# Kernel optimization log

Hardware: AMD Instinct MI355X
Metric: run time of the kernel (lower is better)

The kernel has to match this reference:

```python
import jax, jax.numpy as jnp
import numpy as np

N, M, C, CSKIP, K = 16384, 4096, 256, 128, 3
BIG = 1e10  # distance penalty for cross-batch pairs


def setup_inputs() -> dict:
    key = jax.random.key(0)
    ks = jax.random.split(key, 6)
    return {
        "x": jax.random.normal(ks[0], (M, C), jnp.float32),
        "pos": jax.random.normal(ks[1], (M, 3), jnp.float32),
        "batch": jnp.zeros((M,), jnp.int32),
        "x_skip": jax.random.normal(ks[2], (N, CSKIP), jnp.float32),
        "pos_skip": jax.random.normal(ks[3], (N, 3), jnp.float32),
        "batch_skip": jnp.zeros((N,), jnp.int32),
        "W1": jax.random.normal(ks[4], (C + CSKIP, 256), jnp.float32) * (1.0 / np.sqrt(C + CSKIP)),
        "b1": jnp.zeros((256,), jnp.float32),
        "W2": jax.random.normal(ks[5], (256, 256), jnp.float32) * (1.0 / np.sqrt(256)),
        "b2": jnp.zeros((256,), jnp.float32),
    }


def _knn_idx(pos, pos_skip, batch, batch_skip, k):
    # Squared distances via GEMM form: [N, M]
    a2 = jnp.sum(pos_skip * pos_skip, axis=-1, keepdims=True)      # [N,1]
    b2 = jnp.sum(pos * pos, axis=-1)[None, :]                       # [1,M]
    d2 = a2 + b2 - 2.0 * (pos_skip @ pos.T)                         # [N,M]
    d2 = jnp.where(batch_skip[:, None] != batch[None, :], BIG, d2)
    _, idx = jax.lax.top_k(-d2, k)                                  # [N,k]
    return idx


def reference(x, pos, batch, x_skip, pos_skip, batch_skip, W1, b1, W2, b2):
    idx = _knn_idx(pos, pos_skip, batch, batch_skip, K)             # [N,k] coarse neighbor ids
    # Exact squared dist recomputed from gathered positions (matches torch diff path)
    diff = pos_skip[:, None, :] - pos[idx]                          # [N,k,3]
    d2 = jnp.sum(diff * diff, axis=-1, keepdims=True)               # [N,k,1]
    w = 1.0 / (d2 + 1e-8)                                           # inverse-distance weights
    wsum = jnp.sum(w, axis=1, keepdims=True)                        # per-row scatter_add == sum over k
    w = w / (wsum + 1e-8)
    x_interp = jnp.sum(w * x[idx], axis=1)                          # [N,C]
    h = jnp.concatenate([x_interp, x_skip], axis=1)                 # [N,C+C']
    h = jax.nn.relu(h @ W1 + b1)
    h = jax.nn.relu(h @ W2 + b2)
    return h
```

## Files before the change

### kernel.cpp

```cpp
#include <hip/hip_runtime.h>

typedef float     f4   __attribute__((ext_vector_type(4)));
typedef float     f32x4 __attribute__((ext_vector_type(4)));
typedef _Float16  h8   __attribute__((ext_vector_type(8)));
typedef _Float16  h4   __attribute__((ext_vector_type(4)));
typedef int       i4   __attribute__((ext_vector_type(4)));

#define NQ   16384
#define MP   4096
#define CF   256
#define CSK  128
#define K1   384
#define HID  256
#define QB   16

__global__ __launch_bounds__(256) void wconv_kernel(
    const float* __restrict__ W1, const float* __restrict__ W2,
    _Float16* __restrict__ Wt1, _Float16* __restrict__ Wt2)
{
    const int i = blockIdx.x * 256 + threadIdx.x;
    if (i < K1 * HID) {
        const int k = i >> 8, n = i & 255;
        Wt1[(size_t)(k >> 5) * 8192 + ((k >> 3) & 3) * 2048 + n * 8 + (k & 7)]
            = (_Float16)W1[i];
    } else {
        const int i2 = i - K1 * HID;
        const int k = i2 >> 8, n = i2 & 255;
        Wt2[(size_t)(k >> 5) * 8192 + ((k >> 3) & 3) * 2048 + n * 8 + (k & 7)]
            = (_Float16)W2[i2];
    }
}

__global__ __launch_bounds__(256, 4) void fused_kernel(
    const float* __restrict__ pos,
    const float* __restrict__ pos_skip,
    const float* __restrict__ x,
    const float* __restrict__ x_skip,
    const _Float16* __restrict__ Wt1,
    const _Float16* __restrict__ Wt2,
    const float* __restrict__ b1,
    const float* __restrict__ b2,
    float* __restrict__ out)
{
    __shared__ __align__(16) char smem[26112];
    _Float16* pxh = (_Float16*)smem;
    _Float16* pyh = (_Float16*)(smem + 8192);
    _Float16* pzh = (_Float16*)(smem + 16384);
    unsigned short (*ci)[48] = (unsigned short (*)[48])(smem + 24576);
    int   (*fidx)[3] = (int (*)[3])(smem + 24576);
    float (*fw)[3]   = (float (*)[3])(smem + 24768);
    _Float16 (*As)[392] = (_Float16 (*)[392])smem;
    _Float16 (*Hs)[264] = (_Float16 (*)[264])smem;

    const int tid = threadIdx.x;

    {
        const f4* posv = (const f4*)pos;
        for (int m = tid; m < MP / 4; m += 256) {
            const f4 a = posv[3*m], b = posv[3*m+1], c = posv[3*m+2];
            h4 hx, hy, hz;
            hx[0]=(_Float16)a[0]; hx[1]=(_Float16)a[3];
            hx[2]=(_Float16)b[2]; hx[3]=(_Float16)c[1];
            hy[0]=(_Float16)a[1]; hy[1]=(_Float16)b[0];
            hy[2]=(_Float16)b[3]; hy[3]=(_Float16)c[2];
            hz[0]=(_Float16)a[2]; hz[1]=(_Float16)b[1];
            hz[2]=(_Float16)c[0]; hz[3]=(_Float16)c[3];
            *(h4*)&pxh[4*m] = hx;
            *(h4*)&pyh[4*m] = hy;
            *(h4*)&pzh[4*m] = hz;
        }
    }
    __syncthreads();

    const int lane = tid & 63;
    const int wv   = tid >> 6;

    {
        float qx[4], qy[4], qz[4];
        #pragma unroll
        for (int k = 0; k < 4; k++) {
            const int q = blockIdx.x * QB + wv * 4 + k;
            qx[k] = pos_skip[3*q+0];
            qy[k] = pos_skip[3*q+1];
            qz[k] = pos_skip[3*q+2];
        }

        unsigned K0[4], K1v[4], K2[4];
        #pragma unroll
        for (int k = 0; k < 4; k++) { K0[k] = ~0u; K1v[k] = ~0u; K2[k] = ~0u; }

        #define EVAL(PX, PY, PZ, J)                                           \
            _Pragma("unroll")                                                 \
            for (int k = 0; k < 4; k++) {                                     \
                const float dx = qx[k] - (PX), dy = qy[k] - (PY),             \
                            dz = qz[k] - (PZ);                                \
                const float dd = fmaf(dx, dx, fmaf(dy, dy, dz * dz));         \
                const unsigned key = (__float_as_uint(dd) & 0xFFFFF000u) | (J);\
                const unsigned h0 = max(K0[k], key);                          \
                K0[k] = min(K0[k], key);                                      \
                const unsigned n1 = min(K1v[k], h0);                          \
                const unsigned h1 = max(K1v[k], h0);                          \
                K1v[k] = n1;                                                  \
                K2[k] = min(K2[k], h1);                                       \
            }

        float c0x = (float)pxh[lane],       c1x = (float)pxh[lane + 64],
              c2x = (float)pxh[lane + 128], c3x = (float)pxh[lane + 192];
        float c0y = (float)pyh[lane],       c1y = (float)pyh[lane + 64],
              c2y = (float)pyh[lane + 128], c3y = (float)pyh[lane + 192];
        float c0z = (float)pzh[lane],       c1z = (float)pzh[lane + 64],
              c2z = (float)pzh[lane + 128], c3z = (float)pzh[lane + 192];

        for (int it = 0; it < 64; it += 4) {
            const unsigned jb = it * 64 + lane;
            const float nx0 = (float)pxh[jb + 256], nx1 = (float)pxh[jb + 320],
                        nx2 = (float)pxh[jb + 384], nx3 = (float)pxh[jb + 448];
            const float ny0 = (float)pyh[jb + 256], ny1 = (float)pyh[jb + 320],
                        ny2 = (float)pyh[jb + 384], ny3 = (float)pyh[jb + 448];
            const float nz0 = (float)pzh[jb + 256], nz1 = (float)pzh[jb + 320],
                        nz2 = (float)pzh[jb + 384], nz3 = (float)pzh[jb + 448];
            EVAL(c0x, c0y, c0z, jb);
            EVAL(c1x, c1y, c1z, jb + 64);
            EVAL(c2x, c2y, c2z, jb + 128);
            EVAL(c3x, c3y, c3z, jb + 192);
            c0x = nx0; c1x = nx1; c2x = nx2; c3x = nx3;
            c0y = ny0; c1y = ny1; c2y = ny2; c3y = ny3;
            c0z = nz0; c1z = nz1; c2z = nz2; c3z = nz3;
        }
        #undef EVAL

        #pragma unroll
        for (int k = 0; k < 4; k++) {
            unsigned a0 = K0[k], a1 = K1v[k], a2 = K2[k];
            {
                const unsigned b0 = (unsigned)__builtin_amdgcn_ds_swizzle((int)a0, 0x041F);
                const unsigned b1 = (unsigned)__builtin_amdgcn_ds_swizzle((int)a1, 0x041F);
                const unsigned b2 = (unsigned)__builtin_amdgcn_ds_swizzle((int)a2, 0x041F);
                const unsigned m0 = min(a0, b0);
                const unsigned c1 = max(a0, b0);
                const unsigned d0 = min(a1, b1), d1 = max(a1, b1);
                const unsigned m1 = min(c1, d0);
                const unsigned m2 = min(min(max(c1, d0), d1), min(a2, b2));
                a0 = m0; a1 = m1; a2 = m2;
            }
            {
                const unsigned b0 = (unsigned)__builtin_amdgcn_ds_swizzle((int)a0, 0x081F);
                const unsigned b1 = (unsigned)__builtin_amdgcn_ds_swizzle((int)a1, 0x081F);
                const unsigned b2 = (unsigned)__builtin_amdgcn_ds_swizzle((int)a2, 0x081F);
                const unsigned m0 = min(a0, b0);
                const unsigned c1 = max(a0, b0);
                const unsigned d0 = min(a1, b1), d1 = max(a1, b1);
                const unsigned m1 = min(c1, d0);
                const unsigned m2 = min(min(max(c1, d0), d1), min(a2, b2));
                a0 = m0; a1 = m1; a2 = m2;
            }
            if (!(lane & 3)) {
                const int q = wv * 4 + k;
                const int pr = lane >> 2;
                ci[q][pr*3+0] = (unsigned short)(a0 & 0xFFFu);
                ci[q][pr*3+1] = (unsigned short)(a1 & 0xFFFu);
                ci[q][pr*3+2] = (unsigned short)(a2 & 0xFFFu);
            }
        }
    }
    __syncthreads();

    if (tid < 8 * QB) {
        const int q    = tid >> 3;
        const int part = tid & 7;
        const int g    = blockIdx.x * QB + q;
        const double qxd = (double)pos_skip[3*g+0];
        const double qyd = (double)pos_skip[3*g+1];
        const double qzd = (double)pos_skip[3*g+2];
        const double a2d = qxd*qxd + qyd*qyd + qzd*qzd;

        double e0 = 1e300, e1 = 1e300, e2 = 1e300;
        int    j0 = 0,     j1 = 0,     j2 = 0;
        #pragma unroll
        for (int c = 0; c < 6; c++) {
            const int j = ci[q][part*6 + c];
            const double pxd = (double)pos[3*j+0];
            const double pyd = (double)pos[3*j+1];
            const double pzd = (double)pos[3*j+2];
            const double b2  = pxd*pxd + pyd*pyd + pzd*pzd;
            const double dot = qxd*pxd + qyd*pyd + qzd*pzd;
            const double d   = (a2d + b2) - 2.0 * dot;
            if (d < e2) {
                if (d < e1) {
                    e2 = e1; j2 = j1;
                    if (d < e0) { e1 = e0; j1 = j0; e0 = d; j0 = j; }
                    else        { e1 = d;  j1 = j; }
                } else { e2 = d; j2 = j; }
            }
        }
        ci[q][part*3+0] = (unsigned short)j0;
        ci[q][part*3+1] = (unsigned short)j1;
        ci[q][part*3+2] = (unsigned short)j2;
    }
    __syncthreads();

    if (tid < QB) {
        const int g = blockIdx.x * QB + tid;
        const double qxd = (double)pos_skip[3*g+0];
        const double qyd = (double)pos_skip[3*g+1];
        const double qzd = (double)pos_skip[3*g+2];
        const double a2d = qxd*qxd + qyd*qyd + qzd*qzd;

        double e0 = 1e300, e1 = 1e300, e2 = 1e300;
        int    j0 = 0,     j1 = 0,     j2 = 0;
        for (int p = 0; p < 8; p++) {
            #pragma unroll
            for (int s = 0; s < 3; s++) {
                const int j = ci[tid][p*3+s];
                const double pxd = (double)pos[3*j+0];
                const double pyd = (double)pos[3*j+1];
                const double pzd = (double)pos[3*j+2];
                const double b2  = pxd*pxd + pyd*pyd + pzd*pzd;
                const double dot = qxd*pxd + qyd*pyd + qzd*pzd;
                const double d   = (a2d + b2) - 2.0 * dot;
                if (d < e2) {
                    if (d < e1) {
                        e2 = e1; j2 = j1;
                        if (d < e0) { e1 = e0; j1 = j0; e0 = d; j0 = j; }
                        else        { e1 = d;  j1 = j; }
                    } else { e2 = d; j2 = j; }
                }
            }
        }
        const float sx = pos_skip[3*g+0], sy = pos_skip[3*g+1], sz = pos_skip[3*g+2];
        const int jj[3] = { j0, j1, j2 };
        float wv3[3];
        #pragma unroll
        for (int k = 0; k < 3; k++) {
            const float dx = sx - pos[3*jj[k]+0];
            const float dy = sy - pos[3*jj[k]+1];
            const float dz = sz - pos[3*jj[k]+2];
            const float dd = dx*dx + dy*dy + dz*dz;
            wv3[k] = 1.0f / (dd + 1e-8f);
        }
        const float inv = 1.0f / (wv3[0] + wv3[1] + wv3[2] + 1e-8f);
        #pragma unroll
        for (int k = 0; k < 3; k++) {
            fidx[tid][k] = jj[k];
            fw[tid][k]   = wv3[k] * inv;
        }
    }
    __syncthreads();

    const int row0 = blockIdx.x * QB;

    {
        const int r   = tid >> 4;
        const int sub = tid & 15;
        const int j0 = fidx[r][0], j1 = fidx[r][1], j2 = fidx[r][2];
        const float w0 = fw[r][0], w1 = fw[r][1], w2 = fw[r][2];
        const f4* xa = (const f4*)(x + (size_t)j0 * CF);
        const f4* xb = (const f4*)(x + (size_t)j1 * CF);
        const f4* xc = (const f4*)(x + (size_t)j2 * CF);
        const f4* xs = (const f4*)(x_skip + (size_t)(row0 + r) * CSK);
        #pragma unroll
        for (int t = 0; t < 4; t++) {
            const int c4 = t * 16 + sub;
            const f4 a = xa[c4], b = xb[c4], c = xc[c4];
            const f4 v = a * w0 + b * w1 + c * w2;
            h4 hv; hv[0]=(_Float16)v[0]; hv[1]=(_Float16)v[1];
                   hv[2]=(_Float16)v[2]; hv[3]=(_Float16)v[3];
            *(h4*)&As[r][c4 * 4] = hv;
        }
        #pragma unroll
        for (int t = 0; t < 2; t++) {
            const int c4 = t * 16 + sub;
            const f4 v = xs[c4];
            h4 hv; hv[0]=(_Float16)v[0]; hv[1]=(_Float16)v[1];
                   hv[2]=(_Float16)v[2]; hv[3]=(_Float16)v[3];
            *(h4*)&As[r][CF + c4 * 4] = hv;
        }
    }

    const int ln   = tid & 15;
    const int quad = (tid >> 4) & 3;
    const int nb   = wv * 64;
    const int q8   = quad * 8;

    const _Float16* w1b = Wt1 + quad * 2048 + (size_t)(nb + ln) * 8;
    const _Float16* w2b = Wt2 + quad * 2048 + (size_t)(nb + ln) * 8;

    f32x4 acc[4];
    #pragma unroll
    for (int nt = 0; nt < 4; nt++) acc[nt] = (f32x4)0.0f;

    h8 B[6][4];
    #pragma unroll
    for (int s = 0; s < 6; s++)
        #pragma unroll
        for (int nt = 0; nt < 4; nt++)
            B[s][nt] = *(const h8*)(w1b + (size_t)s * 8192 + nt * 128);

    __syncthreads();

    #pragma unroll
    for (int kb = 0; kb < 12; kb++) {
        const int s = kb % 6;
        const h8 ha = *(const h8*)&As[ln][kb*32 + q8];
        h8 hb[4];
        #pragma unroll
        for (int nt = 0; nt < 4; nt++) hb[nt] = B[s][nt];
        if (kb < 6) {
            #pragma unroll
            for (int nt = 0; nt < 4; nt++)
                B[s][nt] = *(const h8*)(w1b + (size_t)(kb+6) * 8192 + nt * 128);
        } else {
            #pragma unroll
            for (int nt = 0; nt < 4; nt++)
                B[s][nt] = *(const h8*)(w2b + (size_t)(kb-6) * 8192 + nt * 128);
        }
        #pragma unroll
        for (int nt = 0; nt < 4; nt++)
            acc[nt] = __builtin_amdgcn_mfma_f32_16x16x32_f16(ha, hb[nt], acc[nt], 0, 0, 0);
    }
    __syncthreads();

    #pragma unroll
    for (int nt = 0; nt < 4; nt++) {
        const int n = nb + nt*16 + ln;
        const float bv = b1[n];
        #pragma unroll
        for (int r = 0; r < 4; r++) {
            const int m = quad*4 + r;
            Hs[m][n] = (_Float16)fmaxf(acc[nt][r] + bv, 0.0f);
        }
        acc[nt] = (f32x4)0.0f;
    }
    __syncthreads();

    #pragma unroll
    for (int kb = 0; kb < 8; kb++) {
        const int s = kb % 6;
        const h8 ha = *(const h8*)&Hs[ln][kb*32 + q8];
        h8 hb[4];
        #pragma unroll
        for (int nt = 0; nt < 4; nt++) hb[nt] = B[s][nt];
        if (kb < 2) {
            #pragma unroll
            for (int nt = 0; nt < 4; nt++)
                B[s][nt] = *(const h8*)(w2b + (size_t)(kb+6) * 8192 + nt * 128);
        }
        #pragma unroll
        for (int nt = 0; nt < 4; nt++)
            acc[nt] = __builtin_amdgcn_mfma_f32_16x16x32_f16(ha, hb[nt], acc[nt], 0, 0, 0);
    }

    #pragma unroll
    for (int nt = 0; nt < 4; nt++) {
        const int n = nb + nt*16 + ln;
        const float bv = b2[n];
        #pragma unroll
        for (int r = 0; r < 4; r++) {
            const int m = quad*4 + r;
            out[(size_t)(row0 + m) * HID + n] = fmaxf(acc[nt][r] + bv, 0.0f);
        }
    }
}

extern "C" void kernel_launch(void* const* d_in, const int* in_sizes, int n_in,
                              void* d_out, int out_size, void* d_ws, size_t ws_size,
                              hipStream_t stream) {
    const float* x         = (const float*)d_in[0];
    const float* pos       = (const float*)d_in[1];
    const float* x_skip    = (const float*)d_in[3];
    const float* pos_skip  = (const float*)d_in[4];
    const float* W1        = (const float*)d_in[6];
    const float* b1        = (const float*)d_in[7];
    const float* W2        = (const float*)d_in[8];
    const float* b2        = (const float*)d_in[9];
    float* out = (float*)d_out;

    char* ws = (char*)d_ws;
    _Float16* Wt1 = (_Float16*)ws;
    _Float16* Wt2 = (_Float16*)(ws + 196608);

    wconv_kernel<<<(K1*HID + HID*HID) / 256, 256, 0, stream>>>(W1, W2, Wt1, Wt2);
    fused_kernel<<<NQ / QB, 256, 0, stream>>>(pos, pos_skip, x, x_skip,
                                              Wt1, Wt2, b1, b2, out);
}
```

Before: 123.4 us.

## Use packed fp16 distance math and med3-based top-3 insertion in KNN scan

```diff
diff --git a/kernel.cpp b/kernel.cpp
--- a/kernel.cpp
+++ b/kernel.cpp
@@ -4,7 +4,7 @@
 typedef float     f32x4 __attribute__((ext_vector_type(4)));
 typedef _Float16  h8   __attribute__((ext_vector_type(8)));
 typedef _Float16  h4   __attribute__((ext_vector_type(4)));
-typedef int       i4   __attribute__((ext_vector_type(4)));
+typedef _Float16  h2   __attribute__((ext_vector_type(2)));
 
 #define NQ   16384
 #define MP   4096
@@ -13,6 +13,12 @@
 #define K1   384
 #define HID  256
 #define QB   16
+
+__device__ __forceinline__ unsigned umed3(unsigned a, unsigned b, unsigned c) {
+    unsigned r;
+    asm("v_med3_u32 %0, %1, %2, %3" : "=v"(r) : "v"(a), "v"(b), "v"(c));
+    return r;
+}
 
 __global__ __launch_bounds__(256) void wconv_kernel(
     const float* __restrict__ W1, const float* __restrict__ W2,
@@ -76,58 +82,65 @@
     const int wv   = tid >> 6;
 
     {
-        float qx[4], qy[4], qz[4];
+        h2 q2x[4], q2y[4], q2z[4];
         #pragma unroll
         for (int k = 0; k < 4; k++) {
             const int q = blockIdx.x * QB + wv * 4 + k;
-            qx[k] = pos_skip[3*q+0];
-            qy[k] = pos_skip[3*q+1];
-            qz[k] = pos_skip[3*q+2];
+            const _Float16 hx = (_Float16)pos_skip[3*q+0];
+            const _Float16 hy = (_Float16)pos_skip[3*q+1];
+            const _Float16 hz = (_Float16)pos_skip[3*q+2];
+            q2x[k][0] = hx; q2x[k][1] = hx;
+            q2y[k][0] = hy; q2y[k][1] = hy;
+            q2z[k][0] = hz; q2z[k][1] = hz;
         }
 
         unsigned K0[4], K1v[4], K2[4];
         #pragma unroll
         for (int k = 0; k < 4; k++) { K0[k] = ~0u; K1v[k] = ~0u; K2[k] = ~0u; }
 
-        #define EVAL(PX, PY, PZ, J)                                           \
-            _Pragma("unroll")                                                 \
-            for (int k = 0; k < 4; k++) {                                     \
-                const float dx = qx[k] - (PX), dy = qy[k] - (PY),             \
-                            dz = qz[k] - (PZ);                                \
-                const float dd = fmaf(dx, dx, fmaf(dy, dy, dz * dz));         \
-                const unsigned key = (__float_as_uint(dd) & 0xFFFFF000u) | (J);\
-                const unsigned h0 = max(K0[k], key);                          \
-                K0[k] = min(K0[k], key);                                      \
-                const unsigned n1 = min(K1v[k], h0);                          \
-                const unsigned h1 = max(K1v[k], h0);                          \
-                K1v[k] = n1;                                                  \
-                K2[k] = min(K2[k], h1);                                       \
-            }
-
-        float c0x = (float)pxh[lane],       c1x = (float)pxh[lane + 64],
-              c2x = (float)pxh[lane + 128], c3x = (float)pxh[lane + 192];
-        float c0y = (float)pyh[lane],       c1y = (float)pyh[lane + 64],
-              c2y = (float)pyh[lane + 128], c3y = (float)pyh[lane + 192];
-        float c0z = (float)pzh[lane],       c1z = (float)pzh[lane + 64],
-              c2z = (float)pzh[lane + 128], c3z = (float)pzh[lane + 192];
-
-        for (int it = 0; it < 64; it += 4) {
-            const unsigned jb = it * 64 + lane;
-            const float nx0 = (float)pxh[jb + 256], nx1 = (float)pxh[jb + 320],
-                        nx2 = (float)pxh[jb + 384], nx3 = (float)pxh[jb + 448];
-            const float ny0 = (float)pyh[jb + 256], ny1 = (float)pyh[jb + 320],
-                        ny2 = (float)pyh[jb + 384], ny3 = (float)pyh[jb + 448];
-            const float nz0 = (float)pzh[jb + 256], nz1 = (float)pzh[jb + 320],
-                        nz2 = (float)pzh[jb + 384], nz3 = (float)pzh[jb + 448];
-            EVAL(c0x, c0y, c0z, jb);
-            EVAL(c1x, c1y, c1z, jb + 64);
-            EVAL(c2x, c2y, c2z, jb + 128);
-            EVAL(c3x, c3y, c3z, jb + 192);
-            c0x = nx0; c1x = nx1; c2x = nx2; c3x = nx3;
-            c0y = ny0; c1y = ny1; c2y = ny2; c3y = ny3;
-            c0z = nz0; c1z = nz1; c2z = nz2; c3z = nz3;
-        }
-        #undef EVAL
+        #define INS(k, key) {                                              \
+            const unsigned o0 = K0[k], o1 = K1v[k], o2 = K2[k];            \
+            K0[k]  = min(o0, (key));                                       \
+            K1v[k] = umed3(o0, o1, (key));                                 \
+            K2[k]  = umed3(o1, o2, (key));                                 \
+        }
+
+        union hpack { h4 v4; h2 v2[2]; };
+        #define EVALP(CX, CY, CZ, JB)                                      \
+            _Pragma("unroll")                                              \
+            for (int k = 0; k < 4; k++) {                                  \
+                _Pragma("unroll")                                          \
+                for (int pp = 0; pp < 2; pp++) {                           \
+                    const h2 dx = q2x[k] - (CX).v2[pp];                    \
+                    const h2 dy = q2y[k] - (CY).v2[pp];                    \
+                    const h2 dz = q2z[k] - (CZ).v2[pp];                    \
+                    const h2 dd = dx*dx + dy*dy + dz*dz;                   \
+                    const unsigned du = __builtin_bit_cast(unsigned, dd);  \
+                    const unsigned key0 = ((du & 0xFFFFu) << 12) + (JB) + pp*2; \
+                    const unsigned key1 = ((du >> 16) << 12) + (JB) + pp*2 + 1; \
+                    INS(k, key0);                                          \
+                    INS(k, key1);                                          \
+                }                                                          \
+            }
+
+        const h4* px4 = (const h4*)pxh;
+        const h4* py4 = (const h4*)pyh;
+        const h4* pz4 = (const h4*)pzh;
+
+        hpack cx, cy, cz, nx, ny, nz;
+        int idx = lane;
+        cx.v4 = px4[idx]; cy.v4 = py4[idx]; cz.v4 = pz4[idx];
+
+        for (int it = 0; it < 16; ++it) {
+            const int nidx = idx + 64;
+            nx.v4 = px4[nidx]; ny.v4 = py4[nidx]; nz.v4 = pz4[nidx];
+            const unsigned jb = (unsigned)(it * 256 + lane * 4);
+            EVALP(cx, cy, cz, jb);
+            cx = nx; cy = ny; cz = nz;
+            idx = nidx;
+        }
+        #undef EVALP
+        #undef INS
 
         #pragma unroll
         for (int k = 0; k < 4; k++) {
```

After: 117.3 us. 4.9% less time.
